# Optimization experiments

Measured on AMD Instinct MI355X. Metric: run time of the kernel, lower is better.

Reference implementation:

```python
import jax, jax.numpy as jnp
import numpy as np
import math

B, T, C = 4, 1024, 1024
H = 16          # n_head
E = 8           # num_experts
K = 2           # top_k
HID = 4096      # expert_hidden_dim
TEMP = 1.0
EPS_LN = 1e-5


def setup_inputs() -> dict:
    key = jax.random.key(0)
    ks = jax.random.split(key, 16)
    s = 0.02
    return {
        'x': jax.random.normal(ks[0], (B, T, C), jnp.float32),
        'ln1_g': jnp.ones((C,), jnp.float32),
        'ln1_b': jnp.zeros((C,), jnp.float32),
        'W_qkv': jax.random.normal(ks[1], (C, 3 * C), jnp.float32) * s,
        'b_qkv': jnp.zeros((3 * C,), jnp.float32),
        'W_proj': jax.random.normal(ks[2], (C, C), jnp.float32) * s,
        'b_proj': jnp.zeros((C,), jnp.float32),
        'ln2_g': jnp.ones((C,), jnp.float32),
        'ln2_b': jnp.zeros((C,), jnp.float32),
        'W_router': jax.random.normal(ks[3], (C, E), jnp.float32) * s,
        'W1': jax.random.normal(ks[4], (E, C, HID), jnp.float32) * s,
        'b1': jnp.zeros((E, HID), jnp.float32),
        'W2': jax.random.normal(ks[5], (E, HID, C), jnp.float32) * s,
        'b2': jnp.zeros((E, C), jnp.float32),
    }


def _layernorm(x, g, b):
    mu = jnp.mean(x, axis=-1, keepdims=True)
    var = jnp.mean(jnp.square(x - mu), axis=-1, keepdims=True)
    return (x - mu) * jax.lax.rsqrt(var + EPS_LN) * g + b


def reference(x, ln1_g, ln1_b, W_qkv, b_qkv, W_proj, b_proj,
              ln2_g, ln2_b, W_router, W1, b1, W2, b2):
    D = C // H
    # --- causal self-attention on ln_1(x) ---
    h = _layernorm(x, ln1_g, ln1_b)
    qkv = h @ W_qkv + b_qkv                      # [B,T,3C]
    q, k, v = jnp.split(qkv, 3, axis=-1)
    q = q.reshape(B, T, H, D).transpose(0, 2, 1, 3)   # [B,H,T,D]
    k = k.reshape(B, T, H, D).transpose(0, 2, 1, 3)
    v = v.reshape(B, T, H, D).transpose(0, 2, 1, 3)
    att = jnp.einsum('bhqd,bhkd->bhqk', q, k) * (1.0 / math.sqrt(D))
    mask = jnp.tril(jnp.ones((T, T), bool))
    att = jnp.where(mask, att, -jnp.inf)
    att = jax.nn.softmax(att, axis=-1)
    y = jnp.einsum('bhqk,bhkd->bhqd', att, v)
    y = y.transpose(0, 2, 1, 3).reshape(B, T, C)
    x = x + (y @ W_proj + b_proj)

    # --- sparse MoE on ln_2(x) ---
    h2 = _layernorm(x, ln2_g, ln2_b)
    xf = h2.reshape(-1, C)                       # [N,C]
    N = xf.shape[0]
    logits = (xf @ W_router) / TEMP              # [N,E]
    prob = jax.nn.softmax(logits, axis=-1)
    top_prob, top_idx = jax.lax.top_k(prob, K)   # [N,K]
    top_prob = top_prob / (jnp.sum(top_prob, axis=-1, keepdims=True) + 1e-9)
    # dense per-token per-expert combine weights (0 for unselected experts)
    w = jnp.zeros((N, E), xf.dtype).at[jnp.arange(N)[:, None], top_idx].add(top_prob)
    # dense expert compute (weights zero out unselected experts -> same math)
    hid = jax.nn.gelu(jnp.einsum('nc,ech->neh', xf, W1) + b1, approximate=False)
    eo = jnp.einsum('neh,ehc->nec', hid, W2) + b2          # [N,E,C]
    out_flat = jnp.einsum('nec,ne->nc', eo, w)
    x = x + out_flat.reshape(B, T, C)

    counts = jnp.zeros((E,), jnp.float32).at[top_idx.reshape(-1)].add(1.0)
    expert_utilization = counts / (jnp.sum(counts) + 1e-9)
    return x, expert_utilization
```

## Files before the change

kernel.cpp:

```cpp
#include <hip/hip_runtime.h>
#include <cmath>

#define CDIM 1024
#define NTOK 4096
#define NHEAD 16
#define HDIM 64
#define NEXP 8
#define HIDD 4096
#define MAXROWS 9216

typedef short bf16x8 __attribute__((ext_vector_type(8)));
typedef short s16x4  __attribute__((ext_vector_type(4)));
typedef float f32x4  __attribute__((ext_vector_type(4)));

static __device__ __forceinline__ short f2bf(float f){
  unsigned u = __builtin_bit_cast(unsigned, f);
  u += 0x7fffu + ((u >> 16) & 1u);
  return (short)(u >> 16);
}
static __device__ __forceinline__ float bf2f(short s){
  unsigned u = ((unsigned)(unsigned short)s) << 16;
  return __builtin_bit_cast(float, u);
}
static __device__ __forceinline__ float gelu_t(float x){
  const float y = 0.7978845608f*(x + 0.044715f*x*x*x);
  const float e = __expf(2.f*y);
  return 0.5f*x*(1.f + (e-1.f)/(e+1.f));
}

static __device__ __forceinline__ int swz64(int r, int ch){
  return r*64 + (((ch ^ (r>>1)) & 3) << 4);
}
static __device__ __forceinline__ int swz128(int r, int ch){
  return r*128 + (((ch ^ r) & 7) << 4);
}

static __device__ __forceinline__ void gl16(const short* g, short* l){
  __builtin_amdgcn_global_load_lds(
      (const __attribute__((address_space(1))) void*)g,
      (__attribute__((address_space(3))) void*)l, 16, 0, 0);
}

__global__ void k_transpose_all(const float* __restrict__ Wqkv, const float* __restrict__ Wproj,
                                const float* __restrict__ W1, const float* __restrict__ W2,
                                short* __restrict__ WtQ, short* __restrict__ WtP,
                                short* __restrict__ Wt1, short* __restrict__ Wt2){
  const int id = blockIdx.x;
  const float* src; short* dst; int R, Cc, bx, by;
  if (id < 768){
    src = Wqkv; dst = WtQ; R = 1024; Cc = 3072;
    bx = id % 48; by = id / 48;
  } else if (id < 1024){
    const int t = id - 768;
    src = Wproj; dst = WtP; R = 1024; Cc = 1024;
    bx = t % 16; by = t / 16;
  } else if (id < 9216){
    const int t = id - 1024, z = t >> 10, tt = t & 1023;
    src = W1 + (long long)z*1024*4096; dst = Wt1 + (long long)z*1024*4096;
    R = 1024; Cc = 4096;
    bx = tt % 64; by = tt / 64;
  } else {
    const int t = id - 9216, z = t >> 10, tt = t & 1023;
    src = W2 + (long long)z*4096*1024; dst = Wt2 + (long long)z*4096*1024;
    R = 4096; Cc = 1024;
    bx = tt % 16; by = tt / 16;
  }
  __shared__ float tile[64][65];
  const int r0 = by*64, c0 = bx*64;
  const int t = threadIdx.x;
  #pragma unroll
  for (int it=0; it<4; ++it){
    const int item = t + it*256;
    const int r = item>>4, c4 = item&15;
    const float4 v = *(const float4*)(src + (long long)(r0+r)*Cc + c0 + c4*4);
    tile[r][c4*4+0]=v.x; tile[r][c4*4+1]=v.y; tile[r][c4*4+2]=v.z; tile[r][c4*4+3]=v.w;
  }
  __syncthreads();
  #pragma unroll
  for (int it=0; it<2; ++it){
    const int item = t + it*256;
    const int rr8 = item & 7, cc = item >> 3;
    bf16x8 o;
    #pragma unroll
    for (int i=0;i<8;i++) o[i] = f2bf(tile[rr8*8+i][cc]);
    *(bf16x8*)(dst + (long long)(c0+cc)*R + r0 + rr8*8) = o;
  }
}

__global__ void k_ln1(const float* __restrict__ x, const float* __restrict__ g,
                      const float* __restrict__ b, short* __restrict__ out,
                      int* __restrict__ counts, int* __restrict__ curs,
                      int* __restrict__ zrowi, int* __restrict__ rowmap){
  const int row = blockIdx.x;
  const int t = threadIdx.x;
  const int gid = row*256 + t;
  if (gid < 2048) zrowi[gid] = 0;
  if (gid < MAXROWS) rowmap[gid] = -1;
  if (gid < 8){ counts[gid] = 0; curs[gid] = 0; }

  const float4 v = ((const float4*)(x + (long long)row*CDIM))[t];
  float s  = v.x+v.y+v.z+v.w;
  float s2 = v.x*v.x+v.y*v.y+v.z*v.z+v.w*v.w;
  #pragma unroll
  for (int mm=1; mm<64; mm<<=1){ s += __shfl_xor(s,mm); s2 += __shfl_xor(s2,mm); }
  __shared__ float ps[4], ps2[4];
  const int w = t>>6, l = t&63;
  if (l==0){ ps[w]=s; ps2[w]=s2; }
  __syncthreads();
  s  = ps[0]+ps[1]+ps[2]+ps[3];
  s2 = ps2[0]+ps2[1]+ps2[2]+ps2[3];
  const float mu = s*(1.f/CDIM);
  const float rstd = rsqrtf(s2*(1.f/CDIM) - mu*mu + 1e-5f);
  const float4 gg = ((const float4*)g)[t];
  const float4 bb = ((const float4*)b)[t];
  s16x4 o;
  o[0]=f2bf((v.x-mu)*rstd*gg.x+bb.x); o[1]=f2bf((v.y-mu)*rstd*gg.y+bb.y);
  o[2]=f2bf((v.z-mu)*rstd*gg.z+bb.z); o[3]=f2bf((v.w-mu)*rstd*gg.w+bb.w);
  *(s16x4*)(out + (long long)row*CDIM + t*4) = o;
}

__global__ void k_ln2_router(const float* __restrict__ x1, const float* __restrict__ g,
                             const float* __restrict__ b, const float* __restrict__ Wr,
                             short* __restrict__ h2, int* __restrict__ tidx,
                             float* __restrict__ tw, int* __restrict__ counts){
  const int row = blockIdx.x;
  const int t = threadIdx.x;
  const float4 v = ((const float4*)(x1 + (long long)row*CDIM))[t];
  float s  = v.x+v.y+v.z+v.w;
  float s2 = v.x*v.x+v.y*v.y+v.z*v.z+v.w*v.w;
  #pragma unroll
  for (int mm=1; mm<64; mm<<=1){ s += __shfl_xor(s,mm); s2 += __shfl_xor(s2,mm); }
  __shared__ float ps[4], ps2[4];
  const int w = t>>6, l = t&63;
  if (l==0){ ps[w]=s; ps2[w]=s2; }
  __syncthreads();
  s  = ps[0]+ps[1]+ps[2]+ps[3];
  s2 = ps2[0]+ps2[1]+ps2[2]+ps2[3];
  const float mu = s*(1.f/CDIM);
  const float rstd = rsqrtf(s2*(1.f/CDIM) - mu*mu + 1e-5f);
  const float4 gg = ((const float4*)g)[t];
  const float4 bb = ((const float4*)b)[t];
  const float y0=(v.x-mu)*rstd*gg.x+bb.x, y1=(v.y-mu)*rstd*gg.y+bb.y;
  const float y2=(v.z-mu)*rstd*gg.z+bb.z, y3=(v.w-mu)*rstd*gg.w+bb.w;
  s16x4 o; o[0]=f2bf(y0); o[1]=f2bf(y1); o[2]=f2bf(y2); o[3]=f2bf(y3);
  *(s16x4*)(h2 + (long long)row*CDIM + t*4) = o;

  float acc[8];
  const float* wr0 = Wr + (long long)(t*4)*NEXP;
  #pragma unroll
  for (int e=0;e<8;e++) acc[e] = y0*wr0[e] + y1*wr0[8+e] + y2*wr0[16+e] + y3*wr0[24+e];
  #pragma unroll
  for (int mm=1; mm<64; mm<<=1){
    #pragma unroll
    for (int e=0;e<8;e++) acc[e] += __shfl_xor(acc[e], mm);
  }
  __shared__ float pl[4][8];
  if (l==0){
    #pragma unroll
    for (int e=0;e<8;e++) pl[w][e]=acc[e];
  }
  __syncthreads();
  if (t==0){
    float lg[8];
    #pragma unroll
    for (int e=0;e<8;e++) lg[e] = pl[0][e]+pl[1][e]+pl[2][e]+pl[3][e];
    float mx = lg[0];
    #pragma unroll
    for (int e=1;e<8;e++) mx = fmaxf(mx, lg[e]);
    float pr[8]; float sum = 0.f;
    #pragma unroll
    for (int e=0;e<8;e++){ pr[e]=expf(lg[e]-mx); sum += pr[e]; }
    int i0 = 0;
    #pragma unroll
    for (int e=1;e<8;e++) if (pr[e] > pr[i0]) i0 = e;
    int i1 = (i0==0) ? 1 : 0;
    #pragma unroll
    for (int e=0;e<8;e++) if (e!=i0 && pr[e] > pr[i1]) i1 = e;
    const float p0 = pr[i0]/sum, p1 = pr[i1]/sum;
    const float dn = p0 + p1 + 1e-9f;
    tidx[row*2]=i0; tidx[row*2+1]=i1;
    tw[row*2]=p0/dn; tw[row*2+1]=p1/dn;
    atomicAdd(&counts[i0],1); atomicAdd(&counts[i1],1);
  }
}

__global__ void k_scatter(const int* __restrict__ tidx, const float* __restrict__ tw,
                          const int* __restrict__ counts, int* __restrict__ curs0,
                          int* __restrict__ offs, float* __restrict__ util,
                          int* __restrict__ rowmap, float* __restrict__ roww,
                          int* __restrict__ posmap){
  __shared__ int soff[9];
  if (threadIdx.x == 0){
    int o = 0;
    for (int e=0;e<8;e++){
      soff[e] = o;
      o += (counts[e] + 127) & ~127;
    }
    soff[8] = o;
    if (blockIdx.x == 0){
      for (int e=0;e<9;e++) offs[e] = soff[e];
      for (int e=0;e<8;e++) util[e] = (float)counts[e] / 8192.0f;
    }
  }
  __syncthreads();
  const int i = blockIdx.x*blockDim.x + threadIdx.x;
  if (i >= 2*NTOK) return;
  const int e = tidx[i];
  const int pos = soff[e] + atomicAdd(&curs0[e], 1);
  rowmap[pos] = i >> 1;
  roww[pos]   = tw[i];
  posmap[i]   = pos;
}

template<int EPI>
__launch_bounds__(512, 4)
__global__ void k_gemm(const short* __restrict__ A, const short* __restrict__ Bt,
                       const float* __restrict__ bias, const float* __restrict__ resid,
                       void* __restrict__ Cout, int N, int K,
                       const int* __restrict__ rowmap, const int* __restrict__ offs,
                       long long expStrideB, const short* __restrict__ zrow){
  int wg = blockIdx.x;
  const int nwg = gridDim.x;
  {
    const int q = nwg >> 3, r8 = nwg & 7;
    const int xcd = wg & 7, pos = wg >> 3;
    wg = (xcd < r8 ? xcd*(q+1) : r8*(q+1) + (xcd - r8)*q) + pos;
  }
  const int gridN = N >> 7;
  const int mtile = wg / gridN, ntile = wg % gridN;
  const int mbase = mtile*128;
  const int nbase = ntile*128;
  int e = 0;
  if constexpr (EPI >= 2){
    if (mbase >= offs[8]) return;
    while (e < 7 && mbase >= offs[e+1]) e++;
    Bt += (long long)e * expStrideB;
  }
  __shared__ short Asm[2][4096];
  __shared__ short Bsm[2][4096];
  const int tid = threadIdx.x;
  const int w = tid >> 6, l = tid & 63;
  const int wr = w >> 1, wc = w & 1;
  const int l15 = l & 15, l4 = l >> 4;

  const short* aSrc; const short* bSrc;
  {
    const int r = tid >> 2, ch = tid & 3;
    const int sch = (ch ^ (r >> 1)) & 3;
    if constexpr (EPI == 2){
      const int grow = rowmap[mbase + r];
      aSrc = (grow >= 0) ? (A + (long long)grow*K + sch*8) : (zrow + sch*8);
    } else {
      aSrc = A + (long long)(mbase + r)*K + sch*8;
    }
    bSrc = Bt + (long long)(nbase + r)*K + sch*8;
  }
  const int dOff = w*512;

  f32x4 acc[2][4];
  const f32x4 z4 = {0.f,0.f,0.f,0.f};
  #pragma unroll
  for (int i=0;i<2;i++){
    #pragma unroll
    for (int jn=0;jn<4;jn++) acc[i][jn] = z4;
  }

  auto stage = [&](int buf, int kt){
    gl16(aSrc + kt, &Asm[buf][dOff]);
    gl16(bSrc + kt, &Bsm[buf][dOff]);
  };
  auto compute = [&](int buf){
    bf16x8 af[2], bfr[4];
    #pragma unroll
    for (int i=0;i<2;i++)
      af[i]  = *(const bf16x8*)((char*)Asm[buf] + swz64(wr*32 + i*16 + l15, l4));
    #pragma unroll
    for (int jn=0;jn<4;jn++)
      bfr[jn] = *(const bf16x8*)((char*)Bsm[buf] + swz64(wc*64 + jn*16 + l15, l4));
    #pragma unroll
    for (int i=0;i<2;i++){
      #pragma unroll
      for (int jn=0;jn<4;jn++)
        acc[i][jn] = __builtin_amdgcn_mfma_f32_16x16x32_bf16(af[i], bfr[jn], acc[i][jn], 0,0,0);
    }
  };

  stage(0, 0);
  asm volatile("s_waitcnt vmcnt(0)" ::: "memory");
  __builtin_amdgcn_s_barrier();

  int cur = 0;
  for (int kt = 32; kt < K; kt += 32){
    stage(cur ^ 1, kt);
    compute(cur);
    asm volatile("s_waitcnt vmcnt(0)" ::: "memory");
    __builtin_amdgcn_s_barrier();
    cur ^= 1;
  }
  compute(cur);

  #pragma unroll
  for (int i=0;i<2;i++){
    const int row0 = mbase + wr*32 + i*16 + l4*4;
    #pragma unroll
    for (int jn=0;jn<4;jn++){
      const int col = nbase + wc*64 + jn*16 + l15;
      const float bi = bias[(EPI>=2 ? e*N : 0) + col];
      #pragma unroll
      for (int j=0;j<4;j++){
        const long long idx = (long long)(row0 + j)*N + col;
        float v = acc[i][jn][j] + bi;
        if constexpr (EPI == 0){
          ((short*)Cout)[idx] = f2bf(v);
        } else if constexpr (EPI == 1){
          ((float*)Cout)[idx] = v + resid[idx];
        } else if constexpr (EPI == 2){
          ((short*)Cout)[idx] = f2bf(gelu_t(v));
        } else {
          ((short*)Cout)[idx] = f2bf(v);
        }
      }
    }
  }
}

__launch_bounds__(512)
__global__ void k_attn(const short* __restrict__ qkv, short* __restrict__ y){
  const int qp = blockIdx.x;
  const int bh = blockIdx.y;
  const int bb = bh >> 4;
  const int h  = bh & 15;
  const int tid = threadIdx.x;
  const int w = tid >> 6, l = tid & 63;
  const int half = w >> 2, wq = w & 3;
  const int l15 = l & 15, l4 = l >> 4;

  __shared__ short Ksm[128*64];
  __shared__ short Vtsm[64*128];
  __shared__ short Psm[8*16*64];

  const long long rs = 3*CDIM;
  const int qrow0 = bb*1024 + qp*128;
  const int myQt = (qp << 1) + half;

  bf16x8 aq[2];
  {
    const int qr = qrow0 + half*64 + wq*16 + l15;
    const short* qp2 = qkv + (long long)qr*rs + h*HDIM;
    aq[0] = *(const bf16x8*)(qp2 + l4*8);
    aq[1] = *(const bf16x8*)(qp2 + 32 + l4*8);
  }

  const f32x4 z4 = {0.f,0.f,0.f,0.f};
  f32x4 O[4];
  #pragma unroll
  for (int cf=0;cf<4;cf++) O[cf] = z4;
  float mrow[4], lrow[4];
  #pragma unroll
  for (int j=0;j<4;j++){ mrow[j] = -1e30f; lrow[j] = 0.f; }

  for (int it = 0; it <= qp; ++it){
    const int kvrow0 = bb*1024 + it*128;
    #pragma unroll
    for (int pz=0; pz<2; ++pz){
      const int rr = (tid >> 3) + pz*64;
      const int c = tid & 7;
      const short* kp = qkv + (long long)(kvrow0 + rr)*rs + CDIM + h*HDIM + c*8;
      *(bf16x8*)((char*)Ksm + swz128(rr, c)) = *(const bf16x8*)kp;
      const short* vp = qkv + (long long)(kvrow0 + rr)*rs + 2*CDIM + h*HDIM + c*8;
      bf16x8 vv = *(const bf16x8*)vp;
      #pragma unroll
      for (int i=0;i<8;i++){
        const int d = c*8 + i;
        *(short*)((char*)Vtsm + d*256 + ((((rr>>3) ^ (d&7)) & 15)<<4) + ((2*rr)&15)) = vv[i];
      }
    }
    __syncthreads();

    #pragma unroll
    for (int ks=0; ks<2; ++ks){
      const int kvb = it*2 + ks;
      if (kvb <= myQt){
        f32x4 S[4];
        #pragma unroll
        for (int cf=0;cf<4;cf++) S[cf] = z4;
        #pragma unroll
        for (int cf=0;cf<4;cf++){
          #pragma unroll
          for (int kf=0;kf<2;kf++){
            bf16x8 bk = *(const bf16x8*)((char*)Ksm + swz128(ks*64 + cf*16 + l15, kf*4 + l4));
            S[cf] = __builtin_amdgcn_mfma_f32_16x16x32_bf16(aq[kf], bk, S[cf], 0,0,0);
          }
        }

        const bool diag = (kvb == myQt);
        #pragma unroll
        for (int cf=0;cf<4;cf++){
          #pragma unroll
          for (int j=0;j<4;j++){
            float s = S[cf][j] * 0.125f;
            if (diag && (cf*16 + l15 > wq*16 + l4*4 + j)) s = -1e30f;
            S[cf][j] = s;
          }
        }

        float alpha[4];
        #pragma unroll
        for (int j=0;j<4;j++){
          float mx = fmaxf(fmaxf(S[0][j],S[1][j]), fmaxf(S[2][j],S[3][j]));
          #pragma unroll
          for (int mm=1; mm<16; mm<<=1) mx = fmaxf(mx, __shfl_xor(mx, mm));
          const float mnew = fmaxf(mrow[j], mx);
          const float al = expf(mrow[j] - mnew);
          float psum = 0.f;
          #pragma unroll
          for (int cf=0;cf<4;cf++){ float pp = expf(S[cf][j]-mnew); S[cf][j]=pp; psum += pp; }
          #pragma unroll
          for (int mm=1; mm<16; mm<<=1) psum += __shfl_xor(psum, mm);
          lrow[j] = lrow[j]*al + psum;
          mrow[j] = mnew; alpha[j] = al;
        }
        #pragma unroll
        for (int cf=0;cf<4;cf++){
          #pragma unroll
          for (int j=0;j<4;j++) O[cf][j] *= alpha[j];
        }

        char* pw = (char*)Psm + w*2048;
        #pragma unroll
        for (int cf=0;cf<4;cf++){
          #pragma unroll
          for (int j=0;j<4;j++){
            const int r = l4*4 + j;
            const int cb = (cf*16 + l15)*2;
            *(short*)(pw + r*128 + ((((cb>>4) ^ r) & 7)<<4) + (cb & 15)) = f2bf(S[cf][j]);
          }
        }
        bf16x8 pa[2];
        pa[0] = *(const bf16x8*)(pw + swz128(l15, l4));
        pa[1] = *(const bf16x8*)(pw + swz128(l15, 4 + l4));
        #pragma unroll
        for (int cf=0;cf<4;cf++){
          const int d = cf*16 + l15;
          #pragma unroll
          for (int kf=0;kf<2;kf++){
            const int ch = ks*8 + kf*4 + l4;
            bf16x8 bv = *(const bf16x8*)((char*)Vtsm + d*256 + (((ch ^ (d&7)) & 15)<<4));
            O[cf] = __builtin_amdgcn_mfma_f32_16x16x32_bf16(pa[kf], bv, O[cf], 0,0,0);
          }
        }
      }
    }
    __syncthreads();
  }

  const int yr0 = qrow0 + half*64 + wq*16;
  #pragma unroll
  for (int cf=0;cf<4;cf++){
    #pragma unroll
    for (int j=0;j<4;j++){
      const int r = l4*4 + j;
      y[(long long)(yr0 + r)*CDIM + h*HDIM + cf*16 + l15] = f2bf(O[cf][j] / lrow[j]);
    }
  }
}

__global__ void k_combine(const float* __restrict__ x1, const short* __restrict__ eo,
                          const int* __restrict__ posmap, const float* __restrict__ roww,
                          float* __restrict__ out){
  const int row = blockIdx.x;
  const int t = threadIdx.x;
  const int p0 = posmap[row*2], p1 = posmap[row*2+1];
  const float w0 = roww[p0], w1 = roww[p1];
  const float4 a  = ((const float4*)(x1 + (long long)row*CDIM))[t];
  const s16x4 e0 = *(const s16x4*)(eo + (long long)p0*CDIM + t*4);
  const s16x4 e1 = *(const s16x4*)(eo + (long long)p1*CDIM + t*4);
  float4 r;
  r.x = a.x + w0*bf2f(e0[0]) + w1*bf2f(e1[0]);
  r.y = a.y + w0*bf2f(e0[1]) + w1*bf2f(e1[1]);
  r.z = a.z + w0*bf2f(e0[2]) + w1*bf2f(e1[2]);
  r.w = a.w + w0*bf2f(e0[3]) + w1*bf2f(e1[3]);
  ((float4*)(out + (long long)row*CDIM))[t] = r;
}

extern "C" void kernel_launch(void* const* d_in, const int* in_sizes, int n_in,
                              void* d_out, int out_size, void* d_ws, size_t ws_size,
                              hipStream_t stream){
  const float* x     = (const float*)d_in[0];
  const float* ln1_g = (const float*)d_in[1];
  const float* ln1_b = (const float*)d_in[2];
  const float* W_qkv = (const float*)d_in[3];
  const float* b_qkv = (const float*)d_in[4];
  const float* W_proj= (const float*)d_in[5];
  const float* b_proj= (const float*)d_in[6];
  const float* ln2_g = (const float*)d_in[7];
  const float* ln2_b = (const float*)d_in[8];
  const float* W_r   = (const float*)d_in[9];
  const float* W1    = (const float*)d_in[10];
  const float* b1    = (const float*)d_in[11];
  const float* W2    = (const float*)d_in[12];
  const float* b2    = (const float*)d_in[13];
  float* out = (float*)d_out;
  float* util = out + (long long)NTOK*CDIM;

  char* p = (char*)d_ws;
  auto alloc = [&](size_t bytes)->char*{
    char* r = p; p += (bytes + 255) & ~(size_t)255; return r;
  };
  short* Wt1   = (short*)alloc((size_t)NEXP*HIDD*CDIM*2);
  short* Wt2   = (short*)alloc((size_t)NEXP*CDIM*HIDD*2);
  float* x1    = (float*)alloc((size_t)NTOK*CDIM*4);
  short* h2    = (short*)alloc((size_t)NTOK*CDIM*2);
  short* hid   = (short*)alloc((size_t)MAXROWS*HIDD*2);
  int*   tidx  = (int*)alloc(2*NTOK*4);
  float* tw    = (float*)alloc(2*NTOK*4);
  int*   counts= (int*)alloc(256);
  int*   offs  = (int*)alloc(256);
  int*   curs  = (int*)alloc(256);
  int*   rowmap= (int*)alloc(MAXROWS*4);
  float* roww  = (float*)alloc(MAXROWS*4);
  int*   posmap= (int*)alloc(2*NTOK*4);
  short* zrow  = (short*)alloc(8192);
  char* transStart = p;
  short* WtQ = (short*)alloc((size_t)3*CDIM*CDIM*2);
  short* WtP = (short*)alloc((size_t)CDIM*CDIM*2);
  short* h   = (short*)alloc((size_t)NTOK*CDIM*2);
  short* qkv = (short*)alloc((size_t)NTOK*3*CDIM*2);
  short* y   = (short*)alloc((size_t)NTOK*CDIM*2);
  short* eo  = (short*)transStart;

  k_ln1<<<NTOK, 256, 0, stream>>>(x, ln1_g, ln1_b, h, counts, curs, (int*)zrow, rowmap);

  k_transpose_all<<<17408, 256, 0, stream>>>(W_qkv, W_proj, W1, W2, WtQ, WtP, Wt1, Wt2);

  k_gemm<0><<<dim3((NTOK/128)*(3*CDIM/128)), 512, 0, stream>>>(
      h, WtQ, b_qkv, nullptr, qkv, 3*CDIM, CDIM, nullptr, nullptr, 0, nullptr);

  k_attn<<<dim3(1024/128, 4*NHEAD), 512, 0, stream>>>(qkv, y);

  k_gemm<1><<<dim3((NTOK/128)*(CDIM/128)), 512, 0, stream>>>(
      y, WtP, b_proj, x, x1, CDIM, CDIM, nullptr, nullptr, 0, nullptr);

  k_ln2_router<<<NTOK, 256, 0, stream>>>(x1, ln2_g, ln2_b, W_r, h2, tidx, tw, counts);
  k_scatter<<<(2*NTOK)/256, 256, 0, stream>>>(tidx, tw, counts, curs, offs, util,
                                              rowmap, roww, posmap);

  k_gemm<2><<<dim3((MAXROWS/128)*(HIDD/128)), 512, 0, stream>>>(
      h2, Wt1, b1, nullptr, hid, HIDD, CDIM, rowmap, offs, (long long)HIDD*CDIM, zrow);
  k_gemm<3><<<dim3((MAXROWS/128)*(CDIM/128)), 512, 0, stream>>>(
      hid, Wt2, b2, nullptr, eo, CDIM, HIDD, nullptr, offs, (long long)CDIM*HIDD, zrow);

  k_combine<<<NTOK, 256, 0, stream>>>(x1, eo, posmap, roww, out);
}
```

Before: 595.4 us.

## Prefetch next K/V tile into registers and raise MFMA wave priority in attention

The attention kernel now loads the next iteration's K and V tile from global memory into registers while the current tile is being processed, which overlaps global load latency with compute. The __syncthreads calls are replaced by an explicit lgkmcnt wait plus s_barrier. s_setprio is also raised around the MFMA sections so compute waves get scheduling priority. This costs extra registers, and the second barrier no longer waits on outstanding LDS operations, which could race if a later write reaches shared memory before earlier reads have finished.

```diff
diff --git a/kernel.cpp b/kernel.cpp
--- a/kernel.cpp
+++ b/kernel.cpp
@@ -359,23 +359,35 @@
   #pragma unroll
   for (int j=0;j<4;j++){ mrow[j] = -1e30f; lrow[j] = 0.f; }
 
+  const int srr = tid >> 3, sc = tid & 7;
+  bf16x8 kreg[2], vreg[2];
+  auto gload = [&](int it){
+    const int kvrow0 = bb*1024 + it*128;
+    #pragma unroll
+    for (int pz=0; pz<2; ++pz){
+      const int rr = srr + pz*64;
+      const short* base = qkv + (long long)(kvrow0 + rr)*rs + h*HDIM + sc*8;
+      kreg[pz] = *(const bf16x8*)(base + CDIM);
+      vreg[pz] = *(const bf16x8*)(base + 2*CDIM);
+    }
+  };
+  gload(0);
+
   for (int it = 0; it <= qp; ++it){
-    const int kvrow0 = bb*1024 + it*128;
     #pragma unroll
     for (int pz=0; pz<2; ++pz){
-      const int rr = (tid >> 3) + pz*64;
-      const int c = tid & 7;
-      const short* kp = qkv + (long long)(kvrow0 + rr)*rs + CDIM + h*HDIM + c*8;
-      *(bf16x8*)((char*)Ksm + swz128(rr, c)) = *(const bf16x8*)kp;
-      const short* vp = qkv + (long long)(kvrow0 + rr)*rs + 2*CDIM + h*HDIM + c*8;
-      bf16x8 vv = *(const bf16x8*)vp;
+      const int rr = srr + pz*64;
+      *(bf16x8*)((char*)Ksm + swz128(rr, sc)) = kreg[pz];
+      const bf16x8 vv = vreg[pz];
       #pragma unroll
       for (int i=0;i<8;i++){
-        const int d = c*8 + i;
+        const int d = sc*8 + i;
         *(short*)((char*)Vtsm + d*256 + ((((rr>>3) ^ (d&7)) & 15)<<4) + ((2*rr)&15)) = vv[i];
       }
     }
-    __syncthreads();
+    if (it < qp) gload(it+1);
+    asm volatile("s_waitcnt lgkmcnt(0)" ::: "memory");
+    __builtin_amdgcn_s_barrier();
 
     #pragma unroll
     for (int ks=0; ks<2; ++ks){
@@ -384,6 +396,7 @@
         f32x4 S[4];
         #pragma unroll
         for (int cf=0;cf<4;cf++) S[cf] = z4;
+        __builtin_amdgcn_s_setprio(1);
         #pragma unroll
         for (int cf=0;cf<4;cf++){
           #pragma unroll
@@ -392,6 +405,7 @@
             S[cf] = __builtin_amdgcn_mfma_f32_16x16x32_bf16(aq[kf], bk, S[cf], 0,0,0);
           }
         }
+        __builtin_amdgcn_s_setprio(0);
 
         const bool diag = (kvb == myQt);
         #pragma unroll
@@ -439,6 +453,7 @@
         bf16x8 pa[2];
         pa[0] = *(const bf16x8*)(pw + swz128(l15, l4));
         pa[1] = *(const bf16x8*)(pw + swz128(l15, 4 + l4));
+        __builtin_amdgcn_s_setprio(1);
         #pragma unroll
         for (int cf=0;cf<4;cf++){
           const int d = cf*16 + l15;
@@ -449,9 +464,10 @@
             O[cf] = __builtin_amdgcn_mfma_f32_16x16x32_bf16(pa[kf], bv, O[cf], 0,0,0);
           }
         }
+        __builtin_amdgcn_s_setprio(0);
       }
     }
-    __syncthreads();
+    __builtin_amdgcn_s_barrier();
   }
 
   const int yr0 = qrow0 + half*64 + wq*16;
```

Measured after the change: 609.1 us. +2.3%, slower.
